# Performance work log

Hardware: AMD Instinct MI355X
Metric: run time of the kernel (lower is better)

Reference implementation:

```python
import jax, jax.numpy as jnp
import numpy as np

B, N, IN, H, K, D, L = 8, 1024, 32, 32, 3, 16, 2  # batch, nodes, input_dim, hidden, cheb_k, embed_dim, layers


def setup_inputs() -> dict:
    key = jax.random.key(0)
    ks = jax.random.split(key, 4 + 4 * L)
    inp = {
        "xt": jax.random.normal(ks[0], (B, N, IN), jnp.float32),
        "init_state": jax.random.normal(ks[1], (L, B, N, H), jnp.float32),
        # row-normalized-ish support so the Chebyshev recursion stays bounded
        "support": jax.random.uniform(ks[2], (N, N), jnp.float32) / N,
        "embeddings": jax.random.normal(ks[3], (B, N, D), jnp.float32),
    }
    i = 4
    for l in range(L):
        cin = IN if l == 0 else H
        gi = K * (cin + H)
        inp[f"gate_w{l}"] = jax.random.normal(ks[i], (D, gi, 2 * H), jnp.float32) * (2.0 / (gi + 2 * H)) ** 0.5; i += 1
        inp[f"gate_b{l}"] = jax.random.normal(ks[i], (D, 2 * H), jnp.float32) * 0.05; i += 1
        inp[f"upd_w{l}"] = jax.random.normal(ks[i], (D, gi, H), jnp.float32) * (2.0 / (gi + H)) ** 0.5; i += 1
        inp[f"upd_b{l}"] = jax.random.normal(ks[i], (D, H), jnp.float32) * 0.05; i += 1
    return inp


def _cheb_gconv(x, support, emb, w_pool, b_pool):
    """HimGCN_share forward, meta_axis='ST', 2-D support.
    x: [B,N,C]; support: [N,N]; emb: [B,N,D];
    w_pool: [D, K*C, O]; b_pool: [D, O]. Returns [B,N,O]."""
    n = support.shape[0]
    graphs = [jnp.eye(n, dtype=x.dtype), support]
    for _ in range(2, K):
        graphs.append(2.0 * support @ graphs[-1] - graphs[-2])
    G = jnp.stack(graphs)                                   # [K,N,N]
    c = x.shape[-1]
    x_g = jnp.einsum('knm,bmc->bnkc', G, x).reshape(x.shape[0], n, K * c)  # concat over k
    # faithful to einsum('bni,bnio->bno') with bnio = einsum('bnd,dio->bnio'),
    # contracted in a memory-lighter order (same math)
    xe = jnp.einsum('bni,bnd->bnid', x_g, emb)              # [B,N,K*C,D]
    out = jnp.einsum('bnid,dio->bno', xe, w_pool)
    out = out + jnp.einsum('bnd,do->bno', emb, b_pool)
    return out


def _gcru_cell(x, state, support, emb, gw, gb, uw, ub):
    inp = jnp.concatenate([x, state], axis=-1)
    z_r = jax.nn.sigmoid(_cheb_gconv(inp, support, emb, gw, gb))
    z, r = z_r[..., :H], z_r[..., H:]
    cand = jnp.concatenate([x, z * state], axis=-1)
    hc = jnp.tanh(_cheb_gconv(cand, support, emb, uw, ub))
    return r * state + (1.0 - r) * hc


def reference(xt, init_state, support, embeddings,
              gate_w0, gate_b0, upd_w0, upd_b0,
              gate_w1, gate_b1, upd_w1, upd_b1):
    params = [(gate_w0, gate_b0, upd_w0, upd_b0), (gate_w1, gate_b1, upd_w1, upd_b1)]
    cur = xt
    hidden = []
    for l in range(L):
        gw, gb, uw, ub = params[l]
        cur = _gcru_cell(cur, init_state[l], support, embeddings, gw, gb, uw, ub)
        hidden.append(cur)
    return cur, jnp.stack(hidden)
```

## Files before the change

kernel.cpp:

```cpp
#include <hip/hip_runtime.h>
#include <math.h>

#define BB 8
#define NN 1024
#define HH 32
#define II 192
#define DD 16
#define BN (BB*NN)
#define MT 16
#define FR 512

typedef __attribute__((ext_vector_type(8))) short short8v;
typedef __attribute__((ext_vector_type(4))) float float4v;

union Frag8 { short8v v; uint2 u[2]; uint4 q; };

static __device__ inline ushort bf(float x) {
  union { float f; unsigned u; } c; c.f = x;
  unsigned r = c.u + 0x7FFFu + ((c.u >> 16) & 1u);
  return (ushort)(r >> 16);
}

static __device__ inline uint4 pack8(const ushort e[8]) {
  uint4 v;
  v.x = (unsigned)e[0] | ((unsigned)e[1] << 16);
  v.y = (unsigned)e[2] | ((unsigned)e[3] << 16);
  v.z = (unsigned)e[4] | ((unsigned)e[5] << 16);
  v.w = (unsigned)e[6] | ((unsigned)e[7] << 16);
  return v;
}

template <int O>
static __device__ void prep_w_frag(const float* __restrict__ W,
                                   ushort* __restrict__ WF, int d,
                                   float* lds)
{
  constexpr int NCG = O / 16;
  const float* Wd = W + (size_t)d * II * O;
  ushort* WFd = WF + (size_t)d * NCG * 6 * FR;
  const int tid = threadIdx.x;
  for (int f = tid; f < II * O / 4; f += 256) {
    int i = f / (O / 4);
    int o4 = (f % (O / 4)) * 4;
    float4 v = *(const float4*)(Wd + (size_t)i * O + o4);
    lds[i * (O + 1) + o4 + 0] = v.x; lds[i * (O + 1) + o4 + 1] = v.y;
    lds[i * (O + 1) + o4 + 2] = v.z; lds[i * (O + 1) + o4 + 3] = v.w;
  }
  __syncthreads();
  for (int f = tid; f < NCG * 6 * 64; f += 256) {
    int rem = f % 384;
    int ks = rem >> 6, l = rem & 63;
    int o = (f / 384) * 16 + (l & 15);
    int kb = ks * 32 + (l >> 4) * 4;
    ushort e[8];
#pragma unroll
    for (int j = 0; j < 4; ++j) {
      e[j] = bf(lds[(kb + j) * (O + 1) + o]);
      e[4 + j] = bf(lds[(kb + 16 + j) * (O + 1) + o]);
    }
    *(uint4*)(WFd + (size_t)f * 8) = pack8(e);
  }
}

__global__ __launch_bounds__(256) void prep_all(
    const float* __restrict__ S,
    ushort* __restrict__ SbF, ushort* __restrict__ S2bF,
    const float* __restrict__ gw0, const float* __restrict__ gw1,
    ushort* __restrict__ wfg0, ushort* __restrict__ wfg1,
    const float* __restrict__ uw0, const float* __restrict__ uw1,
    ushort* __restrict__ wfu0, ushort* __restrict__ wfu1,
    const float* __restrict__ xt, const float* __restrict__ st0,
    const float* __restrict__ st1,
    ushort* __restrict__ xbTFg0, ushort* __restrict__ xbTFg1)
{
  union PrepSm {
    float wlds[II * 65];
    struct { ushort A[32][136]; ushort Bt[32][132]; ushort C2[32][36]; } s2;
    ushort T[32 * 72];
  };
  __shared__ PrepSm sm;
  int bx = blockIdx.x;
  const int tid = threadIdx.x;

  if (bx < 1024) {
    const int m0 = (bx >> 5) * 32, n0 = (bx & 31) * 32;
    const int w = tid >> 6, l = tid & 63;
    const int l15 = l & 15, l4 = l >> 4;
    const int wr = (w & 1) * 16, wc = (w >> 1) * 16;

    float4v acc = (float4v){0.f, 0.f, 0.f, 0.f};
    for (int k0 = 0; k0 < NN; k0 += 128) {
      __syncthreads();
#pragma unroll
      for (int q = 0; q < 2; ++q) {
        int f = tid + q * 256;
        int row = f >> 4, s8 = (f & 15) * 8;
        float4 lo = *(const float4*)(S + (size_t)(m0 + row) * NN + k0 + s8);
        float4 hi = *(const float4*)(S + (size_t)(m0 + row) * NN + k0 + s8 + 4);
        sm.s2.A[row][s8 + 0] = bf(lo.x); sm.s2.A[row][s8 + 1] = bf(lo.y);
        sm.s2.A[row][s8 + 2] = bf(lo.z); sm.s2.A[row][s8 + 3] = bf(lo.w);
        sm.s2.A[row][s8 + 4] = bf(hi.x); sm.s2.A[row][s8 + 5] = bf(hi.y);
        sm.s2.A[row][s8 + 6] = bf(hi.z); sm.s2.A[row][s8 + 7] = bf(hi.w);
      }
#pragma unroll
      for (int q = 0; q < 2; ++q) {
        int u = tid + q * 256;
        int kp = u >> 3, c4 = (u & 7) * 4;
        float4 a = *(const float4*)(S + (size_t)(k0 + 2 * kp) * NN + n0 + c4);
        float4 b = *(const float4*)(S + (size_t)(k0 + 2 * kp + 1) * NN + n0 + c4);
        *(unsigned*)&sm.s2.Bt[c4 + 0][2 * kp] = (unsigned)bf(a.x) | ((unsigned)bf(b.x) << 16);
        *(unsigned*)&sm.s2.Bt[c4 + 1][2 * kp] = (unsigned)bf(a.y) | ((unsigned)bf(b.y) << 16);
        *(unsigned*)&sm.s2.Bt[c4 + 2][2 * kp] = (unsigned)bf(a.z) | ((unsigned)bf(b.z) << 16);
        *(unsigned*)&sm.s2.Bt[c4 + 3][2 * kp] = (unsigned)bf(a.w) | ((unsigned)bf(b.w) << 16);
      }
      __syncthreads();
#pragma unroll
      for (int ks = 0; ks < 4; ++ks) {
        int kb = ks * 32 + l4 * 4;
        Frag8 af, bfr;
        af.u[0] = *(const uint2*)&sm.s2.A[wr + l15][kb];
        af.u[1] = *(const uint2*)&sm.s2.A[wr + l15][kb + 16];
        bfr.u[0] = *(const uint2*)&sm.s2.Bt[wc + l15][kb];
        bfr.u[1] = *(const uint2*)&sm.s2.Bt[wc + l15][kb + 16];
        acc = __builtin_amdgcn_mfma_f32_16x16x32_bf16(af.v, bfr.v, acc, 0, 0, 0);
      }
    }
    __syncthreads();
#pragma unroll
    for (int r = 0; r < 4; ++r)
      sm.s2.C2[wr + l4 * 4 + r][wc + l15] = bf(2.f * acc[r]);
    __syncthreads();
    if (tid < 128) {
      int fh = tid >> 6, l2 = tid & 63;
      ushort e[8];
#pragma unroll
      for (int j = 0; j < 4; ++j) {
        e[j] = sm.s2.C2[fh * 16 + (l2 & 15)][(l2 >> 4) * 4 + j];
        e[4 + j] = sm.s2.C2[fh * 16 + (l2 & 15)][(l2 >> 4) * 4 + 16 + j];
      }
      *(uint4*)(S2bF + ((size_t)((bx >> 5) * 2 + fh) * 32 + (bx & 31)) * FR +
                (size_t)l2 * 8) = pack8(e);
    }
    return;
  }
  bx -= 1024;
  if (bx < 32) {
    prep_w_frag<64>(bx >= 16 ? gw1 : gw0, bx >= 16 ? wfg1 : wfg0, bx & 15,
                    sm.wlds);
    return;
  }
  bx -= 32;
  if (bx < 32) {
    prep_w_frag<32>(bx >= 16 ? uw1 : uw0, bx >= 16 ? wfu1 : wfu0, bx & 15,
                    sm.wlds);
    return;
  }
  bx -= 32;
  if (bx < 384) {
    const int tensor = bx / 128, seg = bx % 128;
    const float* src = tensor == 0 ? xt : (tensor == 1 ? st0 : st1);
    ushort* T = sm.T;
    const int n0 = seg * 64;
#pragma unroll
    for (int q = 0; q < 2; ++q) {
      int f = tid + q * 256;
      int n = f >> 3, c4 = (f & 7) * 4;
      float4 v = *(const float4*)(src + (size_t)(n0 + n) * 32 + c4);
      T[(c4 + 0) * 72 + n] = bf(v.x); T[(c4 + 1) * 72 + n] = bf(v.y);
      T[(c4 + 2) * 72 + n] = bf(v.z); T[(c4 + 3) * 72 + n] = bf(v.w);
    }
    __syncthreads();
    {
      int gg = tid >> 7, ksl = (tid >> 6) & 1, l = tid & 63;
      int c = gg * 16 + (l & 15);
      int nb = ksl * 32 + (l >> 4) * 4;
      ushort e[8];
#pragma unroll
      for (int j = 0; j < 4; ++j) {
        e[j] = T[c * 72 + nb + j];
        e[4 + j] = T[c * 72 + nb + 16 + j];
      }
      int b = seg >> 4;
      int ks = (seg & 15) * 2 + ksl;
      ushort* dst; int g;
      if (tensor == 0)      { dst = xbTFg0; g = gg; }
      else if (tensor == 1) { dst = xbTFg0; g = 2 + gg; }
      else                  { dst = xbTFg1; g = 2 + gg; }
      *(uint4*)(dst + (((size_t)b * 4 + g) * 32 + ks) * FR + (size_t)l * 8) =
          pack8(e);
    }
    return;
  }
  bx -= 384;
  {
    const int mt = bx;
#pragma unroll
    for (int q = 0; q < 8; ++q) {
      int f = tid + q * 256;
      int ks = f >> 6, l = f & 63;
      int row = mt * 16 + (l & 15);
      int kb = ks * 32 + (l >> 4) * 4;
      float4 lo = *(const float4*)(S + (size_t)row * NN + kb);
      float4 hi = *(const float4*)(S + (size_t)row * NN + kb + 16);
      ushort e[8] = {bf(lo.x), bf(lo.y), bf(lo.z), bf(lo.w),
                     bf(hi.x), bf(hi.y), bf(hi.z), bf(hi.w)};
      *(uint4*)(SbF + ((size_t)mt * 32 + ks) * FR + (size_t)l * 8) = pack8(e);
    }
  }
}

template <int PHASE>
__global__ __launch_bounds__(512) void gconv_fused(
    const float* __restrict__ xb1,
    const float* __restrict__ xb2,
    const ushort* __restrict__ xbTF,
    const ushort* __restrict__ SbF,
    const ushort* __restrict__ S2bF,
    const float* __restrict__ emb,
    const ushort* __restrict__ WF,
    const float* __restrict__ bias,
    ushort* __restrict__ gT1c,
    float* __restrict__ gT2c,
    float* __restrict__ zr,
    float* __restrict__ zs,
    const float* __restrict__ state,
    float* __restrict__ hid,
    float* __restrict__ outp,
    ushort* __restrict__ xbTFout)
{
  constexpr int O = PHASE == 0 ? 64 : 32;
  constexpr int NCG = O / 16;
  __shared__ ushort A_sm[MT][200];
  __shared__ float emb_sm[MT][17];
  __shared__ float bias_sm[16][64];
  __shared__ float red_sm[4][64][9];

  const int bid = blockIdx.x;
  const int mt = (bid & 7) * 8 + ((bid >> 3) & 7);
  const int b = bid >> 6;
  const int m0 = mt * MT;
  const int tid = threadIdx.x;
  const int w = tid >> 6, l = tid & 63;
  const int cw = w & 3, kh = w >> 2;
  const int l15 = l & 15, l4 = l >> 4;
  const int wcp = (PHASE == 0) ? cw * 16 : (cw & 1) * 16;

  if (tid < MT * 4) {
    int row = tid >> 2, d4 = (tid & 3) * 4;
    float4 v = *(const float4*)(emb + ((size_t)b * NN + m0 + row) * DD + d4);
    emb_sm[row][d4 + 0] = v.x; emb_sm[row][d4 + 1] = v.y;
    emb_sm[row][d4 + 2] = v.z; emb_sm[row][d4 + 3] = v.w;
  }
  for (int f = tid; f < DD * O / 4; f += 512) {
    int d = f / (O / 4), o4 = (f % (O / 4)) * 4;
    *(float4*)&bias_sm[d][o4] = *(const float4*)(bias + (size_t)d * O + o4);
  }
  if (tid < 256) {
    int row = tid >> 4, c4 = (tid & 15) * 4;
    const float* src = (c4 < 32) ? xb1 : xb2;
    float4 v = *(const float4*)(src + ((size_t)b * NN + m0 + row) * 32 + (c4 & 31));
    ushort4 o; o.x = bf(v.x); o.y = bf(v.y); o.z = bf(v.z); o.w = bf(v.w);
    *(ushort4*)&A_sm[row][c4] = o;
  }
  if (PHASE == 1) {
    int row = tid >> 5, c = tid & 31;
    size_t m = (size_t)b * NN + m0 + row;
    A_sm[row][64 + c] = gT1c[m * 32 + c];
    A_sm[row][128 + c] = bf(gT2c[m * 32 + c] - xb1[m * 32 + c]);
  }

  float4v acc1 = (float4v){0.f, 0.f, 0.f, 0.f};
  float4v acc2 = (float4v){0.f, 0.f, 0.f, 0.f};
  {
    const ushort* a1p = SbF + (size_t)mt * 32 * FR + (size_t)l * 8;
    const ushort* a2p = S2bF + (size_t)mt * 32 * FR + (size_t)l * 8;
    const ushort* bp = xbTF +
        (((size_t)b * NCG + (PHASE == 0 ? cw : (cw & 1))) * 32) * FR +
        (size_t)l * 8;
#pragma unroll 4
    for (int ks = kh * 16; ks < kh * 16 + 16; ++ks) {
      Frag8 a1, a2, b0;
      a1.q = *(const uint4*)(a1p + (size_t)ks * FR);
      a2.q = *(const uint4*)(a2p + (size_t)ks * FR);
      b0.q = *(const uint4*)(bp + (size_t)ks * FR);
      acc1 = __builtin_amdgcn_mfma_f32_16x16x32_bf16(a1.v, b0.v, acc1, 0, 0, 0);
      acc2 = __builtin_amdgcn_mfma_f32_16x16x32_bf16(a2.v, b0.v, acc2, 0, 0, 0);
    }
  }

  if (kh == 1) {
#pragma unroll
    for (int j = 0; j < 4; ++j) {
      red_sm[cw][l][j] = acc1[j];
      red_sm[cw][l][4 + j] = acc2[j];
    }
  }
  __syncthreads();
  if (kh == 0) {
#pragma unroll
    for (int j = 0; j < 4; ++j) {
      acc1[j] += red_sm[cw][l][j];
      acc2[j] += red_sm[cw][l][4 + j];
    }
    if (PHASE == 0 && cw < 2) {
#pragma unroll
      for (int r = 0; r < 4; ++r) {
        size_t m = (size_t)b * NN + m0 + l4 * 4 + r;
        gT1c[m * 32 + wcp + l15] = bf(acc1[r]);
        gT2c[m * 32 + wcp + l15] = acc2[r];
      }
    }
    if (PHASE == 0 || cw < 2) {
      const int colX = (PHASE == 0 ? 0 : 32) + wcp + l15;
#pragma unroll
      for (int r = 0; r < 4; ++r) {
        int row = l4 * 4 + r;
        const float* src = (colX < 32) ? xb1 : xb2;
        float xv = src[((size_t)b * NN + m0 + row) * 32 + (colX & 31)];
        A_sm[row][64 + colX] = bf(acc1[r]);
        A_sm[row][128 + colX] = bf(acc2[r] - xv);
      }
    }
  }
  __syncthreads();

  const int cg = (PHASE == 0) ? cw : (cw & 1);
  const int ocol = cg * 16 + l15;
  const int erow = l4 * 4;
  const ushort* wfp = WF + (size_t)cg * 6 * FR + (size_t)l * 8;

  float4v outacc = (float4v){0.f, 0.f, 0.f, 0.f};

#pragma unroll 2
  for (int d = kh * 8; d < kh * 8 + 8; ++d) {
    const ushort* wpd = wfp + (size_t)d * NCG * 6 * FR;
    float4v acc = (float4v){0.f, 0.f, 0.f, 0.f};
#pragma unroll
    for (int ks = 0; ks < 6; ++ks) {
      int kb = ks * 32 + l4 * 4;
      Frag8 af, bfr;
      af.u[0] = *(const uint2*)&A_sm[l15][kb];
      af.u[1] = *(const uint2*)&A_sm[l15][kb + 16];
      bfr.q = *(const uint4*)(wpd + (size_t)ks * FR);
      acc = __builtin_amdgcn_mfma_f32_16x16x32_bf16(af.v, bfr.v, acc, 0, 0, 0);
    }
    float bb = bias_sm[d][ocol];
    outacc[0] += emb_sm[erow + 0][d] * (acc[0] + bb);
    outacc[1] += emb_sm[erow + 1][d] * (acc[1] + bb);
    outacc[2] += emb_sm[erow + 2][d] * (acc[2] + bb);
    outacc[3] += emb_sm[erow + 3][d] * (acc[3] + bb);
  }

  if (kh == 1) {
#pragma unroll
    for (int j = 0; j < 4; ++j) red_sm[cw][l][j] = outacc[j];
  }
  __syncthreads();
  if (kh != 0) return;
#pragma unroll
  for (int j = 0; j < 4; ++j) outacc[j] += red_sm[cw][l][j];

  const int ksn = m0 >> 5;
  const int ebase = (m0 & 16) ? 4 : 0;
  const int lanep = l4 * 16 + (ocol & 15);

  if (PHASE == 0) {
    float zss[4];
#pragma unroll
    for (int r = 0; r < 4; ++r) {
      size_t m = (size_t)b * NN + m0 + erow + r;
      float zv = 1.f / (1.f + __expf(-outacc[r]));
      zr[m * 64 + ocol] = zv;
      if (ocol < 32) {
        float sv = zv * xb2[m * 32 + ocol];
        zs[m * 32 + ocol] = sv;
        zss[r] = sv;
      }
    }
    if (ocol < 32) {
      ushort4 pk; pk.x = bf(zss[0]); pk.y = bf(zss[1]);
      pk.z = bf(zss[2]); pk.w = bf(zss[3]);
      *(ushort4*)(xbTFout + (((size_t)b * 2 + (ocol >> 4)) * 32 + ksn) * FR +
                  (size_t)lanep * 8 + ebase) = pk;
    }
  } else if (cw < 2) {
    float res[4];
#pragma unroll
    for (int r = 0; r < 4; ++r) {
      size_t m = (size_t)b * NN + m0 + erow + r;
      float hc = tanhf(outacc[r]);
      float rg = zr[m * 64 + 32 + ocol];
      float st = state[m * 32 + ocol];
      res[r] = rg * st + (1.f - rg) * hc;
      hid[m * 32 + ocol] = res[r];
      if (outp) outp[m * 32 + ocol] = res[r];
    }
    if (xbTFout) {
      ushort4 pk; pk.x = bf(res[0]); pk.y = bf(res[1]);
      pk.z = bf(res[2]); pk.w = bf(res[3]);
      *(ushort4*)(xbTFout + (((size_t)b * 4 + (ocol >> 4)) * 32 + ksn) * FR +
                  (size_t)lanep * 8 + ebase) = pk;
    }
  }
}

extern "C" void kernel_launch(void* const* d_in, const int* in_sizes, int n_in,
                              void* d_out, int out_size, void* d_ws, size_t ws_size,
                              hipStream_t stream)
{
  const float* xt         = (const float*)d_in[0];
  const float* init_state = (const float*)d_in[1];
  const float* S          = (const float*)d_in[2];
  const float* emb        = (const float*)d_in[3];

  float* out    = (float*)d_out;
  float* hidden = out + (size_t)BN * HH;

  float* zr   = (float*)d_ws;
  float* zs   = zr + (size_t)BN * 64;
  float* gT2c = zs + (size_t)BN * 32;
  ushort* gT1c = (ushort*)(gT2c + (size_t)BN * 32);
  ushort* SbF  = gT1c + (size_t)BN * 32;
  ushort* S2bF = SbF + (size_t)NN * NN;
  ushort* wfg0 = S2bF + (size_t)NN * NN;
  ushort* wfu0 = wfg0 + (size_t)DD * 4 * 6 * FR;
  ushort* wfg1 = wfu0 + (size_t)DD * 2 * 6 * FR;
  ushort* wfu1 = wfg1 + (size_t)DD * 4 * 6 * FR;
  ushort* xbTFg0 = wfu1 + (size_t)DD * 2 * 6 * FR;
  ushort* xbTFu0 = xbTFg0 + (size_t)BB * 4 * 32 * FR;
  ushort* xbTFg1 = xbTFu0 + (size_t)BB * 2 * 32 * FR;
  ushort* xbTFu1 = xbTFg1 + (size_t)BB * 4 * 32 * FR;

  const float* st0 = init_state;
  const float* st1 = init_state + (size_t)BN * HH;
  float* hid0 = hidden;
  float* hid1 = hidden + (size_t)BN * HH;

  prep_all<<<1536, 256, 0, stream>>>(
      S, SbF, S2bF,
      (const float*)d_in[4], (const float*)d_in[8], wfg0, wfg1,
      (const float*)d_in[6], (const float*)d_in[10], wfu0, wfu1,
      xt, st0, st1, xbTFg0, xbTFg1);

  gconv_fused<0><<<512, 512, 0, stream>>>(
      xt, st0, xbTFg0, SbF, S2bF, emb, wfg0, (const float*)d_in[5],
      gT1c, gT2c, zr, zs, nullptr, nullptr, nullptr, xbTFu0);
  gconv_fused<1><<<512, 512, 0, stream>>>(
      xt, zs, xbTFu0, SbF, S2bF, emb, wfu0, (const float*)d_in[7],
      gT1c, gT2c, zr, nullptr, st0, hid0, nullptr, xbTFg1);
  gconv_fused<0><<<512, 512, 0, stream>>>(
      hid0, st1, xbTFg1, SbF, S2bF, emb, wfg1, (const float*)d_in[9],
      gT1c, gT2c, zr, zs, nullptr, nullptr, nullptr, xbTFu1);
  gconv_fused<1><<<512, 512, 0, stream>>>(
      hid0, zs, xbTFu1, SbF, S2bF, emb, wfu1, (const float*)d_in[11],
      gT1c, gT2c, zr, nullptr, st1, hid1, out, nullptr);
}
```

Before: 94.87 us.

## Process 32-row tiles per block to reuse B fragments and weights

Each block now handles two 16-row M tiles (32 nodes) instead of one. The xbTF B-fragment and weight fragments are loaded once and applied to both row tiles with twice the MFMAs. Grid size halves from 512 to 256 blocks. This cuts redundant global loads of B and W per row, but on a 256-CU part it leaves fewer blocks for latency hiding and raises register and LDS use per block.

```diff
diff --git a/kernel.cpp b/kernel.cpp
--- a/kernel.cpp
+++ b/kernel.cpp
@@ -7,7 +7,6 @@
 #define II 192
 #define DD 16
 #define BN (BB*NN)
-#define MT 16
 #define FR 512
 
 typedef __attribute__((ext_vector_type(8))) short short8v;
@@ -230,22 +229,23 @@
 {
   constexpr int O = PHASE == 0 ? 64 : 32;
   constexpr int NCG = O / 16;
-  __shared__ ushort A_sm[MT][200];
-  __shared__ float emb_sm[MT][17];
+  __shared__ ushort A_sm[32][200];
+  __shared__ float emb_sm[32][17];
   __shared__ float bias_sm[16][64];
-  __shared__ float red_sm[4][64][9];
+  __shared__ float red1[4][2][64][4];
+  __shared__ float red2[4][2][64][4];
 
   const int bid = blockIdx.x;
-  const int mt = (bid & 7) * 8 + ((bid >> 3) & 7);
-  const int b = bid >> 6;
-  const int m0 = mt * MT;
+  const int mtp = (bid & 7) * 4 + ((bid >> 3) & 3);
+  const int b = bid >> 5;
+  const int m0 = mtp * 32;
   const int tid = threadIdx.x;
   const int w = tid >> 6, l = tid & 63;
   const int cw = w & 3, kh = w >> 2;
   const int l15 = l & 15, l4 = l >> 4;
   const int wcp = (PHASE == 0) ? cw * 16 : (cw & 1) * 16;
 
-  if (tid < MT * 4) {
+  if (tid < 128) {
     int row = tid >> 2, d4 = (tid & 3) * 4;
     float4 v = *(const float4*)(emb + ((size_t)b * NN + m0 + row) * DD + d4);
     emb_sm[row][d4 + 0] = v.x; emb_sm[row][d4 + 1] = v.y;
@@ -255,7 +255,7 @@
     int d = f / (O / 4), o4 = (f % (O / 4)) * 4;
     *(float4*)&bias_sm[d][o4] = *(const float4*)(bias + (size_t)d * O + o4);
   }
-  if (tid < 256) {
+  {
     int row = tid >> 4, c4 = (tid & 15) * 4;
     const float* src = (c4 < 32) ? xb1 : xb2;
     float4 v = *(const float4*)(src + ((size_t)b * NN + m0 + row) * 32 + (c4 & 31));
@@ -263,63 +263,83 @@
     *(ushort4*)&A_sm[row][c4] = o;
   }
   if (PHASE == 1) {
-    int row = tid >> 5, c = tid & 31;
-    size_t m = (size_t)b * NN + m0 + row;
-    A_sm[row][64 + c] = gT1c[m * 32 + c];
-    A_sm[row][128 + c] = bf(gT2c[m * 32 + c] - xb1[m * 32 + c]);
-  }
-
-  float4v acc1 = (float4v){0.f, 0.f, 0.f, 0.f};
-  float4v acc2 = (float4v){0.f, 0.f, 0.f, 0.f};
+#pragma unroll
+    for (int q = 0; q < 2; ++q) {
+      int e = tid + q * 512;
+      int row = e >> 5, c = e & 31;
+      size_t m = (size_t)b * NN + m0 + row;
+      A_sm[row][64 + c] = gT1c[m * 32 + c];
+      A_sm[row][128 + c] = bf(gT2c[m * 32 + c] - xb1[m * 32 + c]);
+    }
+  }
+
+  float4v acc1[2], acc2[2];
+#pragma unroll
+  for (int rt = 0; rt < 2; ++rt) {
+    acc1[rt] = (float4v){0.f, 0.f, 0.f, 0.f};
+    acc2[rt] = (float4v){0.f, 0.f, 0.f, 0.f};
+  }
   {
-    const ushort* a1p = SbF + (size_t)mt * 32 * FR + (size_t)l * 8;
-    const ushort* a2p = S2bF + (size_t)mt * 32 * FR + (size_t)l * 8;
+    const ushort* a1p0 = SbF + (size_t)(mtp * 2) * 32 * FR + (size_t)l * 8;
+    const ushort* a2p0 = S2bF + (size_t)(mtp * 2) * 32 * FR + (size_t)l * 8;
     const ushort* bp = xbTF +
         (((size_t)b * NCG + (PHASE == 0 ? cw : (cw & 1))) * 32) * FR +
         (size_t)l * 8;
 #pragma unroll 4
     for (int ks = kh * 16; ks < kh * 16 + 16; ++ks) {
-      Frag8 a1, a2, b0;
-      a1.q = *(const uint4*)(a1p + (size_t)ks * FR);
-      a2.q = *(const uint4*)(a2p + (size_t)ks * FR);
+      Frag8 a1r0, a1r1, a2r0, a2r1, b0;
+      a1r0.q = *(const uint4*)(a1p0 + (size_t)ks * FR);
+      a1r1.q = *(const uint4*)(a1p0 + (size_t)(32 + ks) * FR);
+      a2r0.q = *(const uint4*)(a2p0 + (size_t)ks * FR);
+      a2r1.q = *(const uint4*)(a2p0 + (size_t)(32 + ks) * FR);
       b0.q = *(const uint4*)(bp + (size_t)ks * FR);
-      acc1 = __builtin_amdgcn_mfma_f32_16x16x32_bf16(a1.v, b0.v, acc1, 0, 0, 0);
-      acc2 = __builtin_amdgcn_mfma_f32_16x16x32_bf16(a2.v, b0.v, acc2, 0, 0, 0);
+      acc1[0] = __builtin_amdgcn_mfma_f32_16x16x32_bf16(a1r0.v, b0.v, acc1[0], 0, 0, 0);
+      acc1[1] = __builtin_amdgcn_mfma_f32_16x16x32_bf16(a1r1.v, b0.v, acc1[1], 0, 0, 0);
+      acc2[0] = __builtin_amdgcn_mfma_f32_16x16x32_bf16(a2r0.v, b0.v, acc2[0], 0, 0, 0);
+      acc2[1] = __builtin_amdgcn_mfma_f32_16x16x32_bf16(a2r1.v, b0.v, acc2[1], 0, 0, 0);
     }
   }
 
   if (kh == 1) {
 #pragma unroll
-    for (int j = 0; j < 4; ++j) {
-      red_sm[cw][l][j] = acc1[j];
-      red_sm[cw][l][4 + j] = acc2[j];
-    }
+    for (int rt = 0; rt < 2; ++rt)
+#pragma unroll
+      for (int j = 0; j < 4; ++j) {
+        red1[cw][rt][l][j] = acc1[rt][j];
+        red2[cw][rt][l][j] = acc2[rt][j];
+      }
   }
   __syncthreads();
   if (kh == 0) {
 #pragma unroll
-    for (int j = 0; j < 4; ++j) {
-      acc1[j] += red_sm[cw][l][j];
-      acc2[j] += red_sm[cw][l][4 + j];
-    }
+    for (int rt = 0; rt < 2; ++rt)
+#pragma unroll
+      for (int j = 0; j < 4; ++j) {
+        acc1[rt][j] += red1[cw][rt][l][j];
+        acc2[rt][j] += red2[cw][rt][l][j];
+      }
     if (PHASE == 0 && cw < 2) {
 #pragma unroll
-      for (int r = 0; r < 4; ++r) {
-        size_t m = (size_t)b * NN + m0 + l4 * 4 + r;
-        gT1c[m * 32 + wcp + l15] = bf(acc1[r]);
-        gT2c[m * 32 + wcp + l15] = acc2[r];
-      }
+      for (int rt = 0; rt < 2; ++rt)
+#pragma unroll
+        for (int r = 0; r < 4; ++r) {
+          size_t m = (size_t)b * NN + m0 + rt * 16 + l4 * 4 + r;
+          gT1c[m * 32 + wcp + l15] = bf(acc1[rt][r]);
+          gT2c[m * 32 + wcp + l15] = acc2[rt][r];
+        }
     }
     if (PHASE == 0 || cw < 2) {
       const int colX = (PHASE == 0 ? 0 : 32) + wcp + l15;
 #pragma unroll
-      for (int r = 0; r < 4; ++r) {
-        int row = l4 * 4 + r;
-        const float* src = (colX < 32) ? xb1 : xb2;
-        float xv = src[((size_t)b * NN + m0 + row) * 32 + (colX & 31)];
-        A_sm[row][64 + colX] = bf(acc1[r]);
-        A_sm[row][128 + colX] = bf(acc2[r] - xv);
-      }
+      for (int rt = 0; rt < 2; ++rt)
+#pragma unroll
+        for (int r = 0; r < 4; ++r) {
+          int row = rt * 16 + l4 * 4 + r;
+          const float* src = (colX < 32) ? xb1 : xb2;
+          float xv = src[((size_t)b * NN + m0 + row) * 32 + (colX & 31)];
+          A_sm[row][64 + colX] = bf(acc1[rt][r]);
+          A_sm[row][128 + colX] = bf(acc2[rt][r] - xv);
+        }
     }
   }
   __syncthreads();
@@ -329,77 +349,96 @@
   const int erow = l4 * 4;
   const ushort* wfp = WF + (size_t)cg * 6 * FR + (size_t)l * 8;
 
-  float4v outacc = (float4v){0.f, 0.f, 0.f, 0.f};
+  float4v outacc[2];
+  outacc[0] = (float4v){0.f, 0.f, 0.f, 0.f};
+  outacc[1] = (float4v){0.f, 0.f, 0.f, 0.f};
 
 #pragma unroll 2
   for (int d = kh * 8; d < kh * 8 + 8; ++d) {
     const ushort* wpd = wfp + (size_t)d * NCG * 6 * FR;
-    float4v acc = (float4v){0.f, 0.f, 0.f, 0.f};
+    float4v acc[2];
+    acc[0] = (float4v){0.f, 0.f, 0.f, 0.f};
+    acc[1] = (float4v){0.f, 0.f, 0.f, 0.f};
 #pragma unroll
     for (int ks = 0; ks < 6; ++ks) {
       int kb = ks * 32 + l4 * 4;
-      Frag8 af, bfr;
-      af.u[0] = *(const uint2*)&A_sm[l15][kb];
-      af.u[1] = *(const uint2*)&A_sm[l15][kb + 16];
+      Frag8 af0, af1, bfr;
+      af0.u[0] = *(const uint2*)&A_sm[l15][kb];
+      af0.u[1] = *(const uint2*)&A_sm[l15][kb + 16];
+      af1.u[0] = *(const uint2*)&A_sm[16 + l15][kb];
+      af1.u[1] = *(const uint2*)&A_sm[16 + l15][kb + 16];
       bfr.q = *(const uint4*)(wpd + (size_t)ks * FR);
-      acc = __builtin_amdgcn_mfma_f32_16x16x32_bf16(af.v, bfr.v, acc, 0, 0, 0);
+      acc[0] = __builtin_amdgcn_mfma_f32_16x16x32_bf16(af0.v, bfr.v, acc[0], 0, 0, 0);
+      acc[1] = __builtin_amdgcn_mfma_f32_16x16x32_bf16(af1.v, bfr.v, acc[1], 0, 0, 0);
     }
     float bb = bias_sm[d][ocol];
-    outacc[0] += emb_sm[erow + 0][d] * (acc[0] + bb);
-    outacc[1] += emb_sm[erow + 1][d] * (acc[1] + bb);
-    outacc[2] += emb_sm[erow + 2][d] * (acc[2] + bb);
-    outacc[3] += emb_sm[erow + 3][d] * (acc[3] + bb);
+#pragma unroll
+    for (int rt = 0; rt < 2; ++rt) {
+      outacc[rt][0] += emb_sm[rt * 16 + erow + 0][d] * (acc[rt][0] + bb);
+      outacc[rt][1] += emb_sm[rt * 16 + erow + 1][d] * (acc[rt][1] + bb);
+      outacc[rt][2] += emb_sm[rt * 16 + erow + 2][d] * (acc[rt][2] + bb);
+      outacc[rt][3] += emb_sm[rt * 16 + erow + 3][d] * (acc[rt][3] + bb);
+    }
   }
 
   if (kh == 1) {
 #pragma unroll
-    for (int j = 0; j < 4; ++j) red_sm[cw][l][j] = outacc[j];
+    for (int rt = 0; rt < 2; ++rt)
+#pragma unroll
+      for (int j = 0; j < 4; ++j) red1[cw][rt][l][j] = outacc[rt][j];
   }
   __syncthreads();
   if (kh != 0) return;
 #pragma unroll
-  for (int j = 0; j < 4; ++j) outacc[j] += red_sm[cw][l][j];
-
-  const int ksn = m0 >> 5;
-  const int ebase = (m0 & 16) ? 4 : 0;
+  for (int rt = 0; rt < 2; ++rt)
+#pragma unroll
+    for (int j = 0; j < 4; ++j) outacc[rt][j] += red1[cw][rt][l][j];
+
+  const int ksn = mtp;
   const int lanep = l4 * 16 + (ocol & 15);
 
   if (PHASE == 0) {
-    float zss[4];
-#pragma unroll
-    for (int r = 0; r < 4; ++r) {
-      size_t m = (size_t)b * NN + m0 + erow + r;
-      float zv = 1.f / (1.f + __expf(-outacc[r]));
-      zr[m * 64 + ocol] = zv;
+#pragma unroll
+    for (int rt = 0; rt < 2; ++rt) {
+      float zss[4];
+#pragma unroll
+      for (int r = 0; r < 4; ++r) {
+        size_t m = (size_t)b * NN + m0 + rt * 16 + erow + r;
+        float zv = 1.f / (1.f + __expf(-outacc[rt][r]));
+        zr[m * 64 + ocol] = zv;
+        if (ocol < 32) {
+          float sv = zv * xb2[m * 32 + ocol];
+          zs[m * 32 + ocol] = sv;
+          zss[r] = sv;
+        }
+      }
       if (ocol < 32) {
-        float sv = zv * xb2[m * 32 + ocol];
-        zs[m * 32 + ocol] = sv;
-        zss[r] = sv;
-      }
-    }
-    if (ocol < 32) {
-      ushort4 pk; pk.x = bf(zss[0]); pk.y = bf(zss[1]);
-      pk.z = bf(zss[2]); pk.w = bf(zss[3]);
-      *(ushort4*)(xbTFout + (((size_t)b * 2 + (ocol >> 4)) * 32 + ksn) * FR +
-                  (size_t)lanep * 8 + ebase) = pk;
+        ushort4 pk; pk.x = bf(zss[0]); pk.y = bf(zss[1]);
+        pk.z = bf(zss[2]); pk.w = bf(zss[3]);
+        *(ushort4*)(xbTFout + (((size_t)b * 2 + (ocol >> 4)) * 32 + ksn) * FR +
+                    (size_t)lanep * 8 + rt * 4) = pk;
+      }
     }
   } else if (cw < 2) {
-    float res[4];
-#pragma unroll
-    for (int r = 0; r < 4; ++r) {
-      size_t m = (size_t)b * NN + m0 + erow + r;
-      float hc = tanhf(outacc[r]);
-      float rg = zr[m * 64 + 32 + ocol];
-      float st = state[m * 32 + ocol];
-      res[r] = rg * st + (1.f - rg) * hc;
-      hid[m * 32 + ocol] = res[r];
-      if (outp) outp[m * 32 + ocol] = res[r];
-    }
-    if (xbTFout) {
-      ushort4 pk; pk.x = bf(res[0]); pk.y = bf(res[1]);
-      pk.z = bf(res[2]); pk.w = bf(res[3]);
-      *(ushort4*)(xbTFout + (((size_t)b * 4 + (ocol >> 4)) * 32 + ksn) * FR +
-                  (size_t)lanep * 8 + ebase) = pk;
+#pragma unroll
+    for (int rt = 0; rt < 2; ++rt) {
+      float res[4];
+#pragma unroll
+      for (int r = 0; r < 4; ++r) {
+        size_t m = (size_t)b * NN + m0 + rt * 16 + erow + r;
+        float hc = tanhf(outacc[rt][r]);
+        float rg = zr[m * 64 + 32 + ocol];
+        float st = state[m * 32 + ocol];
+        res[r] = rg * st + (1.f - rg) * hc;
+        hid[m * 32 + ocol] = res[r];
+        if (outp) outp[m * 32 + ocol] = res[r];
+      }
+      if (xbTFout) {
+        ushort4 pk; pk.x = bf(res[0]); pk.y = bf(res[1]);
+        pk.z = bf(res[2]); pk.w = bf(res[3]);
+        *(ushort4*)(xbTFout + (((size_t)b * 4 + (ocol >> 4)) * 32 + ksn) * FR +
+                    (size_t)lanep * 8 + rt * 4) = pk;
+      }
     }
   }
 }
@@ -442,16 +481,16 @@
       (const float*)d_in[6], (const float*)d_in[10], wfu0, wfu1,
       xt, st0, st1, xbTFg0, xbTFg1);
 
-  gconv_fused<0><<<512, 512, 0, stream>>>(
+  gconv_fused<0><<<256, 512, 0, stream>>>(
       xt, st0, xbTFg0, SbF, S2bF, emb, wfg0, (const float*)d_in[5],
       gT1c, gT2c, zr, zs, nullptr, nullptr, nullptr, xbTFu0);
-  gconv_fused<1><<<512, 512, 0, stream>>>(
+  gconv_fused<1><<<256, 512, 0, stream>>>(
       xt, zs, xbTFu0, SbF, S2bF, emb, wfu0, (const float*)d_in[7],
       gT1c, gT2c, zr, nullptr, st0, hid0, nullptr, xbTFg1);
-  gconv_fused<0><<<512, 512, 0, stream>>>(
+  gconv_fused<0><<<256, 512, 0, stream>>>(
       hid0, st1, xbTFg1, SbF, S2bF, emb, wfg1, (const float*)d_in[9],
       gT1c, gT2c, zr, zs, nullptr, nullptr, nullptr, xbTFu1);
-  gconv_fused<1><<<512, 512, 0, stream>>>(
+  gconv_fused<1><<<256, 512, 0, stream>>>(
       hid0, zs, xbTFu1, SbF, S2bF, emb, wfu1, (const float*)d_in[11],
       gT1c, gT2c, zr, nullptr, st1, hid1, out, nullptr);
 }
```

Measured after the change: 91.22 us, median of 2. 3.8% less time.
